# Optimization experiments

Measured on AMD Instinct MI355X. Metric: run time of the kernel, lower is better.

The kernel has to match this reference:

```python
import jax, jax.numpy as jnp
import numpy as np

EPS = 1e-9


def _pairwise_sqdist(x1, x2):
    # x1: (B,n,3), x2: (B,m,3) -> (B,n,m) squared euclidean distances
    s1 = jnp.sum(x1 * x1, axis=-1)
    s2 = jnp.sum(x2 * x2, axis=-1)
    cross = jnp.einsum('bnd,bmd->bnm', x1, x2)
    return jnp.maximum(s1[:, :, None] + s2[:, None, :] - 2.0 * cross, 0.0)


def _approxmatch(x1, x2):
    # Faithful port of the approxmatch CUDA kernel (Fan et al. EMD approx).
    B, n, _ = x1.shape
    m = x2.shape[1]
    if n >= m:
        multiL, multiR = 1.0, float(n // m)   # integer division as in CUDA
    else:
        multiL, multiR = float(m // n), 1.0
    dist = _pairwise_sqdist(x1, x2)  # (B,n,m)
    # j = 7 .. -1 -> level = -4^j ; j = -2 -> level = 0  (10 sweeps total)
    levels = jnp.concatenate([
        -(4.0 ** jnp.arange(7, -2, -1, dtype=jnp.float32)),
        jnp.zeros((1,), jnp.float32)])
    match0 = jnp.zeros((B, n, m), jnp.float32)
    remainL0 = jnp.full((B, n), multiL, jnp.float32)
    remainR0 = jnp.full((B, m), multiR, jnp.float32)

    def body(carry, level):
        match, remainL, remainR = carry
        e = jnp.exp(level * dist)                              # (B,n,m)
        suml = EPS + jnp.einsum('bnm,bm->bn', e, remainR)
        ratioL = remainL / suml                                # (B,n)
        sumr = remainR * jnp.einsum('bnm,bn->bm', e, ratioL)   # (B,m)
        consumption = jnp.minimum(remainR / (sumr + EPS), 1.0)
        ratioR = consumption * remainR                         # (B,m)
        remainR = jnp.maximum(0.0, remainR - sumr)
        w = e * ratioL[:, :, None] * ratioR[:, None, :]        # flow k->l
        match = match + w
        remainL = jnp.maximum(0.0, remainL - jnp.sum(w, axis=-1))
        return (match, remainL, remainR), None

    (match, _, _), _ = jax.lax.scan(body, (match0, remainL0, remainR0), levels)
    return match, dist


def setup_inputs() -> dict:
    key = jax.random.key(0)
    k1, k2 = jax.random.split(key)
    B, N = 4, 4096
    xyz1 = jax.random.normal(k1, (B, 3, N), dtype=jnp.float32)
    xyz2 = jax.random.normal(k2, (B, 3, N), dtype=jnp.float32)
    return {"xyz1": xyz1, "xyz2": xyz2}


def reference(xyz1, xyz2):
    # transpose=True: BCN -> BNC
    x1 = jnp.transpose(xyz1, (0, 2, 1))
    x2 = jnp.transpose(xyz2, (0, 2, 1))
    match, dist = _approxmatch(x1, x2)
    d = jnp.sqrt(jnp.maximum(dist, 1e-20))
    cost = jnp.sum(match * d, axis=(1, 2))            # (B,)
    emd = cost / min(x1.shape[1], x2.shape[1])
    return jnp.mean(emd)                               # reduce_mean=True
```

## Files before the change

kernel.cpp:

```cpp
#include <hip/hip_runtime.h>


#define NPTS 4096
#define BATCH 4
#define EMD_EPS 1e-9f
#define TILE 512
#define RPW 4
#define THREADS 256
#define RPB 16
#define NBLK (NPTS / RPB)
#define NBLK_TOTAL (NBLK * BATCH)

#define GRP_SHIFT 4
#define GRP_SIZE (1 << GRP_SHIFT)
#define NGRP (NBLK_TOTAL / GRP_SIZE)
#define BAR_STRIDE 4352
#define NB_BAR 24

#define CULL_FULL -160.0f
#define CULL_PART -40.0f

typedef float v2f __attribute__((ext_vector_type(2)));

struct Params {
    const float* xyz1;
    const float* xyz2;
    float* remainL;
    float* cost_part;
    float* S_L;
    float* out;
    unsigned* bar;
    float* ratioL[10];
    float* ratioR[9];
    float* remainR[9];
    float ls2[10];
};

struct Smem {
    float4 sA[TILE / 2];
    float4 sB[TILE / 2];
    float2 sC[TILE / 2];
    float  s_cost[THREADS / 64];
};

__device__ __forceinline__ float aload(const float* p_) {
    return __hip_atomic_load((float*)p_, __ATOMIC_RELAXED, __HIP_MEMORY_SCOPE_AGENT);
}
__device__ __forceinline__ void astore(float* p_, float v) {
    __hip_atomic_store(p_, v, __ATOMIC_RELAXED, __HIP_MEMORY_SCOPE_AGENT);
}
__device__ __forceinline__ unsigned au_add(unsigned* p_, unsigned v) {
    return __hip_atomic_fetch_add(p_, v, __ATOMIC_RELAXED, __HIP_MEMORY_SCOPE_AGENT);
}
__device__ __forceinline__ unsigned au_load(const unsigned* p_) {
    return __hip_atomic_load((unsigned*)p_, __ATOMIC_RELAXED, __HIP_MEMORY_SCOPE_AGENT);
}
__device__ __forceinline__ void au_store(unsigned* p_, unsigned v) {
    __hip_atomic_store(p_, v, __ATOMIC_RELAXED, __HIP_MEMORY_SCOPE_AGENT);
}

__device__ __forceinline__ void gsync(unsigned* barbase, int idx) {
    __syncthreads();
    if (threadIdx.x == 0) {
        unsigned* B = barbase + idx * BAR_STRIDE;
        const int bid = blockIdx.y * NBLK + blockIdx.x;
        const int grp = bid >> GRP_SHIFT;
        unsigned* gc   = B + grp * 32;
        unsigned* root = B + NGRP * 32;
        unsigned* gr   = B + NGRP * 32 + 32 + grp * 32;
        unsigned old = au_add(gc, 1u);
        if (old == GRP_SIZE - 1u) {
            unsigned r = au_add(root, 1u) + 1u;
            while (r < (unsigned)NGRP) {
                __builtin_amdgcn_s_sleep(4);
                r = au_load(root);
            }
            au_store(gr, 1u);
        } else {
            while (au_load(gr) == 0u)
                __builtin_amdgcn_s_sleep(4);
        }
        asm volatile("" ::: "memory");
    }
    __syncthreads();
}

__device__ __forceinline__ float fexp2(float x) {
#if __has_builtin(__builtin_amdgcn_exp2f)
    return __builtin_amdgcn_exp2f(x);
#else
    return exp2f(x);
#endif
}
__device__ __forceinline__ float fsqrt(float x) {
#if __has_builtin(__builtin_amdgcn_sqrtf)
    return __builtin_amdgcn_sqrtf(x);
#else
    return __sqrtf(x);
#endif
}

__device__ __forceinline__ float wave_reduce(float v) {
    v += __shfl_xor(v, 32);
    v += __shfl_xor(v, 16);
    v += __shfl_xor(v, 8);
    v += __shfl_xor(v, 4);
    v += __shfl_xor(v, 2);
    v += __shfl_xor(v, 1);
    return v;
}

__device__ __forceinline__ void phase_ratioL0(Smem& sm, const Params& p, float ls2,
                                              float* __restrict__ rLout) {
    const int b = blockIdx.y;
    const int tid = threadIdx.x;
    const int wave = tid >> 6;
    const int lane = tid & 63;
    const int row0 = blockIdx.x * RPB + wave * RPW;

    const float* x1 = p.xyz1 + b * 3 * NPTS;
    const float* x2 = p.xyz2 + b * 3 * NPTS;
    const float2* x2x = (const float2*)(x2);
    const float2* x2y = (const float2*)(x2 + NPTS);
    const float2* x2z = (const float2*)(x2 + 2 * NPTS);

    float px[RPW], py[RPW], pz[RPW];
    v2f acc[RPW];
#pragma unroll
    for (int r = 0; r < RPW; ++r) {
        px[r] = x1[row0 + r];
        py[r] = x1[NPTS + row0 + r];
        pz[r] = x1[2 * NPTS + row0 + r];
        acc[r] = (v2f)(0.0f);
    }
    for (int c0 = 0; c0 < NPTS; c0 += TILE) {
        __syncthreads();
        for (int i = tid; i < TILE / 2; i += THREADS) {
            int e = c0 / 2 + i;
            float2 xx = x2x[e], yy = x2y[e];
            sm.sA[i] = make_float4(xx.x, xx.y, yy.x, yy.y);
            sm.sC[i] = x2z[e];
        }
        __syncthreads();
#pragma unroll 2
        for (int j = 0; j < TILE / 128; ++j) {
            float4 a = sm.sA[lane + 64 * j];
            float2 z = sm.sC[lane + 64 * j];
            v2f ax = {a.x, a.y}, ay = {a.z, a.w}, az = {z.x, z.y};
#pragma unroll
            for (int r = 0; r < RPW; ++r) {
                v2f dx = px[r] - ax, dy = py[r] - ay, dz = pz[r] - az;
                v2f d = dx * dx + dy * dy + dz * dz;
                v2f sd = ls2 * d;
                if (!__all(fmaxf(sd.x, sd.y) < CULL_FULL)) {
                    v2f e2 = {fexp2(sd.x), fexp2(sd.y)};
                    acc[r] += e2;
                }
            }
        }
    }
#pragma unroll
    for (int r = 0; r < RPW; ++r) {
        float s = wave_reduce(acc[r].x + acc[r].y);
        if (lane == 0) {
            int idx = b * NPTS + row0 + r;
            astore(&rLout[idx], 1.0f / (EMD_EPS + s));
            p.remainL[idx] = 1.0f;
        }
    }
}

template <bool CULL>
__device__ __forceinline__ void phase_ratioR(Smem& sm, const Params& p, float ls2,
                                             const float* __restrict__ rL,
                                             const float* __restrict__ rRprev,
                                             float* __restrict__ rRout,
                                             float* __restrict__ remROut) {
    const int b = blockIdx.y;
    const int tid = threadIdx.x;
    const int wave = tid >> 6;
    const int lane = tid & 63;
    const int col0 = blockIdx.x * RPB + wave * RPW;

    const float* x1 = p.xyz1 + b * 3 * NPTS;
    const float* x2 = p.xyz2 + b * 3 * NPTS;
    const float2* x1x = (const float2*)(x1);
    const float2* x1y = (const float2*)(x1 + NPTS);
    const float2* x1z = (const float2*)(x1 + 2 * NPTS);
    const float2* wLv = (const float2*)(rL + b * NPTS);

    float px[RPW], py[RPW], pz[RPW];
    v2f acc[RPW];
#pragma unroll
    for (int r = 0; r < RPW; ++r) {
        px[r] = x2[col0 + r];
        py[r] = x2[NPTS + col0 + r];
        pz[r] = x2[2 * NPTS + col0 + r];
        acc[r] = (v2f)(0.0f);
    }
    for (int c0 = 0; c0 < NPTS; c0 += TILE) {
        __syncthreads();
        for (int i = tid; i < TILE / 2; i += THREADS) {
            int e = c0 / 2 + i;
            float2 xx = x1x[e], yy = x1y[e], zz = x1z[e], ww = wLv[e];
            sm.sA[i] = make_float4(xx.x, xx.y, yy.x, yy.y);
            sm.sB[i] = make_float4(zz.x, zz.y, ww.x, ww.y);
        }
        __syncthreads();
#pragma unroll 2
        for (int j = 0; j < TILE / 128; ++j) {
            float4 a = sm.sA[lane + 64 * j];
            float4 bq = sm.sB[lane + 64 * j];
            v2f ax = {a.x, a.y}, ay = {a.z, a.w};
            v2f az = {bq.x, bq.y}, aw = {bq.z, bq.w};
#pragma unroll
            for (int r = 0; r < RPW; ++r) {
                v2f dx = px[r] - ax, dy = py[r] - ay, dz = pz[r] - az;
                v2f d = dx * dx + dy * dy + dz * dz;
                v2f sd = ls2 * d;
                bool live = true;
                if (CULL) live = !__all(fmaxf(sd.x, sd.y) < CULL_FULL);
                if (live) {
                    v2f e2 = {fexp2(sd.x), fexp2(sd.y)};
                    acc[r] += e2 * aw;
                }
            }
        }
    }
#pragma unroll
    for (int r = 0; r < RPW; ++r) {
        float s = wave_reduce(acc[r].x + acc[r].y);
        if (lane == 0) {
            int idx = b * NPTS + col0 + r;
            float rv = rRprev ? rRprev[idx] : 1.0f;
            float sumr = rv * s;
            float cons = fminf(rv / (sumr + EMD_EPS), 1.0f);
            astore(&rRout[idx], cons * rv);
            astore(&remROut[idx], fmaxf(0.0f, rv - sumr));
        }
    }
}

template <bool SQ, bool CULL>
__device__ __forceinline__ void phase_cost(Smem& sm, const Params& p,
                                           float ls2, float ls2n,
                                           const float* __restrict__ rR,
                                           const float* __restrict__ w2,
                                           const float* __restrict__ rLin,
                                           float* __restrict__ rLout,
                                           int initCost) {
    const int b = blockIdx.y;
    const int tid = threadIdx.x;
    const int wave = tid >> 6;
    const int lane = tid & 63;
    const int row0 = blockIdx.x * RPB + wave * RPW;

    const float* x1 = p.xyz1 + b * 3 * NPTS;
    const float* x2 = p.xyz2 + b * 3 * NPTS;
    const float2* x2x = (const float2*)(x2);
    const float2* x2y = (const float2*)(x2 + NPTS);
    const float2* x2z = (const float2*)(x2 + 2 * NPTS);
    const float2* wRv = (const float2*)(rR + b * NPTS);
    const float2* w2v = (const float2*)(w2 + b * NPTS);

    float px[RPW], py[RPW], pz[RPW];
    v2f acc_a[RPW], acc_c[RPW], acc_s[RPW];
#pragma unroll
    for (int r = 0; r < RPW; ++r) {
        px[r] = x1[row0 + r];
        py[r] = x1[NPTS + row0 + r];
        pz[r] = x1[2 * NPTS + row0 + r];
        acc_a[r] = (v2f)(0.0f);
        acc_c[r] = (v2f)(0.0f);
        acc_s[r] = (v2f)(0.0f);
    }
    for (int c0 = 0; c0 < NPTS; c0 += TILE) {
        __syncthreads();
        for (int i = tid; i < TILE / 2; i += THREADS) {
            int e = c0 / 2 + i;
            float2 xx = x2x[e], yy = x2y[e], zz = x2z[e];
            float2 wr = wRv[e];
            float2 cw = w2v[e];
            sm.sA[i] = make_float4(xx.x, xx.y, yy.x, yy.y);
            sm.sB[i] = make_float4(zz.x, zz.y, wr.x, wr.y);
            sm.sC[i] = cw;
        }
        __syncthreads();
#pragma unroll 2
        for (int j = 0; j < TILE / 128; ++j) {
            float4 a = sm.sA[lane + 64 * j];
            float4 bq = sm.sB[lane + 64 * j];
            float2 c = sm.sC[lane + 64 * j];
            v2f ax = {a.x, a.y}, ay = {a.z, a.w};
            v2f az = {bq.x, bq.y}, wr = {bq.z, bq.w};
            v2f cw = {c.x, c.y};
#pragma unroll
            for (int r = 0; r < RPW; ++r) {
                v2f dx = px[r] - ax, dy = py[r] - ay, dz = pz[r] - az;
                v2f d = dx * dx + dy * dy + dz * dz;
                if (SQ) {
                    v2f sd = ls2n * d;
                    bool fullskip = false, partskip = false;
                    if (CULL) {
                        float mx = fmaxf(sd.x, sd.y);
                        fullskip = __all(mx < CULL_FULL);
                        partskip = __all(mx < CULL_PART);
                    }
                    if (!fullskip) {
                        v2f e2 = {fexp2(sd.x), fexp2(sd.y)};
                        acc_s[r] += e2 * cw;
                        if (!partskip) {
                            v2f e4 = e2 * e2;
                            v2f er = (e4 * e4) * wr;
                            acc_a[r] += er;
                            v2f sq = {fsqrt(d.x), fsqrt(d.y)};
                            acc_c[r] += er * sq;
                        }
                    }
                } else {
                    v2f sd = ls2 * d;
                    v2f e1 = {fexp2(sd.x), fexp2(sd.y)};
                    v2f er = e1 * wr;
                    acc_s[r] += cw;
                    acc_a[r] += er;
                    v2f sq = {fsqrt(d.x), fsqrt(d.y)};
                    acc_c[r] += er * sq;
                }
            }
        }
    }
    float wcost = 0.0f;
#pragma unroll
    for (int r = 0; r < RPW; ++r) {
        float sa = wave_reduce(acc_a[r].x + acc_a[r].y);
        float sc = wave_reduce(acc_c[r].x + acc_c[r].y);
        float ss = wave_reduce(acc_s[r].x + acc_s[r].y);
        if (lane == 0) {
            int idx = b * NPTS + row0 + r;
            float rl = rLin[idx];
            float rem = fmaxf(0.0f, p.remainL[idx] - rl * sa);
            p.remainL[idx] = rem;
            astore(&rLout[idx], rem / (EMD_EPS + ss));
            wcost = fmaf(rl, sc, wcost);
        }
    }
    if (lane == 0) sm.s_cost[wave] = wcost;
    __syncthreads();
    if (tid == 0) {
        float t = sm.s_cost[0] + sm.s_cost[1] + sm.s_cost[2] + sm.s_cost[3];
        int ci = b * NBLK + blockIdx.x;
        astore(&p.cost_part[ci], initCost ? t : aload(&p.cost_part[ci]) + t);
    }
}

__device__ __forceinline__ void phase_sum_ratioL(Smem& sm, const Params& p,
                                                 const float* __restrict__ rL) {
    if (blockIdx.x != 0) return;
    const int b = blockIdx.y;
    const int tid = threadIdx.x;
    float s = 0.0f;
    for (int i = tid; i < NPTS; i += 256) s += rL[b * NPTS + i];
    s = wave_reduce(s);
    if ((tid & 63) == 0) sm.s_cost[tid >> 6] = s;
    __syncthreads();
    if (tid == 0)
        astore(&p.S_L[b], sm.s_cost[0] + sm.s_cost[1] + sm.s_cost[2] + sm.s_cost[3]);
}

__device__ __forceinline__ void phase_cost_l0(Smem& sm, const Params& p,
                                              const float* __restrict__ w2,
                                              const float* __restrict__ rL) {
    const int b = blockIdx.y;
    const int tid = threadIdx.x;
    const int wave = tid >> 6;
    const int lane = tid & 63;
    const int row0 = blockIdx.x * RPB + wave * RPW;
    const float sL = aload(&p.S_L[b]);

    const float* x1 = p.xyz1 + b * 3 * NPTS;
    const float* x2 = p.xyz2 + b * 3 * NPTS;
    const float2* x2x = (const float2*)(x2);
    const float2* x2y = (const float2*)(x2 + NPTS);
    const float2* x2z = (const float2*)(x2 + 2 * NPTS);
    const float2* wRv = (const float2*)(w2 + b * NPTS);

    float px[RPW], py[RPW], pz[RPW];
    v2f acc_c[RPW];
#pragma unroll
    for (int r = 0; r < RPW; ++r) {
        px[r] = x1[row0 + r];
        py[r] = x1[NPTS + row0 + r];
        pz[r] = x1[2 * NPTS + row0 + r];
        acc_c[r] = (v2f)(0.0f);
    }
    for (int c0 = 0; c0 < NPTS; c0 += TILE) {
        __syncthreads();
        for (int i = tid; i < TILE / 2; i += THREADS) {
            int e = c0 / 2 + i;
            float2 xx = x2x[e], yy = x2y[e], zz = x2z[e], rv = wRv[e];
            float wr0 = fminf(rv.x / (rv.x * sL + EMD_EPS), 1.0f) * rv.x;
            float wr1 = fminf(rv.y / (rv.y * sL + EMD_EPS), 1.0f) * rv.y;
            sm.sA[i] = make_float4(xx.x, xx.y, yy.x, yy.y);
            sm.sB[i] = make_float4(zz.x, zz.y, wr0, wr1);
        }
        __syncthreads();
#pragma unroll 2
        for (int j = 0; j < TILE / 128; ++j) {
            float4 a = sm.sA[lane + 64 * j];
            float4 bq = sm.sB[lane + 64 * j];
            v2f ax = {a.x, a.y}, ay = {a.z, a.w};
            v2f az = {bq.x, bq.y}, wr = {bq.z, bq.w};
#pragma unroll
            for (int r = 0; r < RPW; ++r) {
                v2f dx = px[r] - ax, dy = py[r] - ay, dz = pz[r] - az;
                v2f d = dx * dx + dy * dy + dz * dz;
                v2f sq = {fsqrt(d.x), fsqrt(d.y)};
                acc_c[r] += wr * sq;
            }
        }
    }
    float wcost = 0.0f;
#pragma unroll
    for (int r = 0; r < RPW; ++r) {
        float sc = wave_reduce(acc_c[r].x + acc_c[r].y);
        if (lane == 0)
            wcost = fmaf(rL[b * NPTS + row0 + r], sc, wcost);
    }
    if (lane == 0) sm.s_cost[wave] = wcost;
    __syncthreads();
    if (tid == 0) {
        float t = sm.s_cost[0] + sm.s_cost[1] + sm.s_cost[2] + sm.s_cost[3];
        int ci = b * NBLK + blockIdx.x;
        astore(&p.cost_part[ci], aload(&p.cost_part[ci]) + t);
    }
}

__device__ __forceinline__ void phase_final(Smem& sm, const Params& p) {
    if (blockIdx.x != 0 || blockIdx.y != 0) return;
    const int tid = threadIdx.x;
    float s = 0.0f;
    for (int i = tid; i < BATCH * NBLK; i += 256) s += aload(&p.cost_part[i]);
    s = wave_reduce(s);
    if ((tid & 63) == 0) sm.s_cost[tid >> 6] = s;
    __syncthreads();
    if (tid == 0)
        p.out[0] = (sm.s_cost[0] + sm.s_cost[1] + sm.s_cost[2] + sm.s_cost[3]) /
                   ((float)NPTS * (float)BATCH);
}

__global__ __launch_bounds__(THREADS, 4) void k_emd_all(Params p) {
    __shared__ Smem sm;
    int bi = 0;
    phase_ratioL0(sm, p, p.ls2[0], p.ratioL[0]);
    gsync(p.bar, bi++);
    for (int t = 0; t < 9; ++t) {
        const float* rRprev = (t == 0) ? nullptr : p.remainR[t - 1];
        if (t < 4)
            phase_ratioR<true>(sm, p, p.ls2[t], p.ratioL[t], rRprev,
                               p.ratioR[t], p.remainR[t]);
        else
            phase_ratioR<false>(sm, p, p.ls2[t], p.ratioL[t], rRprev,
                                p.ratioR[t], p.remainR[t]);
        gsync(p.bar, bi++);
        if (t < 4)
            phase_cost<true, true>(sm, p, p.ls2[t], p.ls2[t + 1], p.ratioR[t],
                                   p.remainR[t], p.ratioL[t], p.ratioL[t + 1], t == 0);
        else if (t < 8)
            phase_cost<true, false>(sm, p, p.ls2[t], p.ls2[t + 1], p.ratioR[t],
                                    p.remainR[t], p.ratioL[t], p.ratioL[t + 1], 0);
        else
            phase_cost<false, false>(sm, p, p.ls2[8], 0.0f, p.ratioR[8],
                                     p.remainR[8], p.ratioL[8], p.ratioL[9], 0);
        gsync(p.bar, bi++);
    }
    phase_sum_ratioL(sm, p, p.ratioL[9]);
    gsync(p.bar, bi++);
    phase_cost_l0(sm, p, p.remainR[8], p.ratioL[9]);
    gsync(p.bar, bi++);
    phase_final(sm, p);
}

__global__ void k_zero(unsigned* bar) {
    const int n = NB_BAR * BAR_STRIDE;
    for (int i = blockIdx.x * 256 + threadIdx.x; i < n; i += gridDim.x * 256)
        __hip_atomic_store(&bar[i], 0u, __ATOMIC_RELAXED, __HIP_MEMORY_SCOPE_AGENT);
}

__global__ __launch_bounds__(THREADS, 4) void kw_ratioL0(Params p) {
    __shared__ Smem sm;
    phase_ratioL0(sm, p, p.ls2[0], p.ratioL[0]);
}
__global__ __launch_bounds__(THREADS, 4) void kw_ratioR(Params p, int t) {
    __shared__ Smem sm;
    const float* rRprev = (t == 0) ? nullptr : p.remainR[t - 1];
    if (t < 4) phase_ratioR<true>(sm, p, p.ls2[t], p.ratioL[t], rRprev,
                                  p.ratioR[t], p.remainR[t]);
    else       phase_ratioR<false>(sm, p, p.ls2[t], p.ratioL[t], rRprev,
                                   p.ratioR[t], p.remainR[t]);
}
__global__ __launch_bounds__(THREADS, 4) void kw_cost(Params p, int t) {
    __shared__ Smem sm;
    if (t < 4)
        phase_cost<true, true>(sm, p, p.ls2[t], p.ls2[t + 1], p.ratioR[t],
                               p.remainR[t], p.ratioL[t], p.ratioL[t + 1], t == 0);
    else if (t < 8)
        phase_cost<true, false>(sm, p, p.ls2[t], p.ls2[t + 1], p.ratioR[t],
                                p.remainR[t], p.ratioL[t], p.ratioL[t + 1], 0);
    else
        phase_cost<false, false>(sm, p, p.ls2[8], 0.0f, p.ratioR[8],
                                 p.remainR[8], p.ratioL[8], p.ratioL[9], 0);
}
__global__ __launch_bounds__(THREADS, 4) void kw_sum(Params p) {
    __shared__ Smem sm;
    phase_sum_ratioL(sm, p, p.ratioL[9]);
}
__global__ __launch_bounds__(THREADS, 4) void kw_cost_l0(Params p) {
    __shared__ Smem sm;
    phase_cost_l0(sm, p, p.remainR[8], p.ratioL[9]);
}
__global__ __launch_bounds__(THREADS, 4) void kw_final(Params p) {
    __shared__ Smem sm;
    phase_final(sm, p);
}

extern "C" void kernel_launch(void* const* d_in, const int* in_sizes, int n_in,
                              void* d_out, int out_size, void* d_ws, size_t ws_size,
                              hipStream_t stream) {
    Params p;
    p.xyz1 = (const float*)d_in[0];
    p.xyz2 = (const float*)d_in[1];
    const int BN = BATCH * NPTS;
    const int BUF = BN + 1024;
    float* ws = (float*)d_ws;
    p.remainL   = ws;
    p.cost_part = ws + BN;
    p.S_L       = p.cost_part + 2048;
    p.bar       = (unsigned*)(p.S_L + 256);
    float* vbase = (float*)(p.bar + NB_BAR * BAR_STRIDE) + 256;
    for (int t = 0; t < 10; ++t) p.ratioL[t]  = vbase + t * BUF;
    for (int t = 0; t < 9; ++t)  p.ratioR[t]  = vbase + (10 + t) * BUF;
    for (int t = 0; t < 9; ++t)  p.remainR[t] = vbase + (19 + t) * BUF;
    p.out = (float*)d_out;

    static const double levels[10] = {
        -16384.0, -4096.0, -1024.0, -256.0, -64.0,
        -16.0, -4.0, -1.0, -0.25, 0.0};
    for (int t = 0; t < 10; ++t)
        p.ls2[t] = (float)(levels[t] * 1.4426950408889634);

    dim3 grid(NBLK, BATCH), blk(THREADS);

    static int coop_ok = -1;
    if (coop_ok < 0) {
        int v = 0;
        hipDeviceGetAttribute(&v, hipDeviceAttributeCooperativeLaunch, 0);
        coop_ok = v;
    }

    hipError_t err = hipErrorUnknown;
    if (coop_ok) {
        k_zero<<<64, 256, 0, stream>>>(p.bar);
        void* args[] = {(void*)&p};
        err = hipLaunchCooperativeKernel((void*)k_emd_all, grid, blk, args, 0, stream);
    }
    if (err != hipSuccess) {
        kw_ratioL0<<<grid, blk, 0, stream>>>(p);
        for (int t = 0; t < 9; ++t) {
            kw_ratioR<<<grid, blk, 0, stream>>>(p, t);
            kw_cost<<<grid, blk, 0, stream>>>(p, t);
        }
        kw_sum<<<dim3(1, BATCH), blk, 0, stream>>>(p);
        kw_cost_l0<<<grid, blk, 0, stream>>>(p);
        kw_final<<<dim3(1, 1), blk, 0, stream>>>(p);
    }
}
```

Measured before the change: 653.0 us.

## Double-buffer shared-memory tiles with register prefetch in all phases

Converts each phase's tile loop to a double-buffered scheme. The next tile's global loads go into registers before computing on the current shared-memory buffer, then the registers are written to the alternate buffer. This hides global load latency behind the exp/sqrt compute and drops one of the two barriers per tile. In exchange it doubles shared memory use and adds register pressure, which may lower occupancy. Its correctness depends on TILE/2 equalling THREADS, since each thread now loads exactly one element.

```diff
diff --git a/kernel.cpp b/kernel.cpp
--- a/kernel.cpp
+++ b/kernel.cpp
@@ -5,6 +5,7 @@
 #define BATCH 4
 #define EMD_EPS 1e-9f
 #define TILE 512
+#define NTILE (NPTS / TILE)
 #define RPW 4
 #define THREADS 256
 #define RPB 16
@@ -37,9 +38,9 @@
 };
 
 struct Smem {
-    float4 sA[TILE / 2];
-    float4 sB[TILE / 2];
-    float2 sC[TILE / 2];
+    float4 sA[2][TILE / 2];
+    float4 sB[2][TILE / 2];
+    float2 sC[2][TILE / 2];
     float  s_cost[THREADS / 64];
 };
 
@@ -133,19 +134,24 @@
         pz[r] = x1[2 * NPTS + row0 + r];
         acc[r] = (v2f)(0.0f);
     }
-    for (int c0 = 0; c0 < NPTS; c0 += TILE) {
-        __syncthreads();
-        for (int i = tid; i < TILE / 2; i += THREADS) {
-            int e = c0 / 2 + i;
-            float2 xx = x2x[e], yy = x2y[e];
-            sm.sA[i] = make_float4(xx.x, xx.y, yy.x, yy.y);
-            sm.sC[i] = x2z[e];
-        }
-        __syncthreads();
+    float2 g0, g1, g2;
+    {
+        int e = tid;
+        g0 = x2x[e]; g1 = x2y[e]; g2 = x2z[e];
+        sm.sA[0][tid] = make_float4(g0.x, g0.y, g1.x, g1.y);
+        sm.sC[0][tid] = g2;
+    }
+    __syncthreads();
+    for (int kt = 0; kt < NTILE; ++kt) {
+        const int cur = kt & 1;
+        if (kt + 1 < NTILE) {
+            int e = (kt + 1) * (TILE / 2) + tid;
+            g0 = x2x[e]; g1 = x2y[e]; g2 = x2z[e];
+        }
 #pragma unroll 2
         for (int j = 0; j < TILE / 128; ++j) {
-            float4 a = sm.sA[lane + 64 * j];
-            float2 z = sm.sC[lane + 64 * j];
+            float4 a = sm.sA[cur][lane + 64 * j];
+            float2 z = sm.sC[cur][lane + 64 * j];
             v2f ax = {a.x, a.y}, ay = {a.z, a.w}, az = {z.x, z.y};
 #pragma unroll
             for (int r = 0; r < RPW; ++r) {
@@ -157,6 +163,11 @@
                     acc[r] += e2;
                 }
             }
+        }
+        if (kt + 1 < NTILE) {
+            sm.sA[cur ^ 1][tid] = make_float4(g0.x, g0.y, g1.x, g1.y);
+            sm.sC[cur ^ 1][tid] = g2;
+            __syncthreads();
         }
     }
 #pragma unroll
@@ -198,19 +209,24 @@
         pz[r] = x2[2 * NPTS + col0 + r];
         acc[r] = (v2f)(0.0f);
     }
-    for (int c0 = 0; c0 < NPTS; c0 += TILE) {
-        __syncthreads();
-        for (int i = tid; i < TILE / 2; i += THREADS) {
-            int e = c0 / 2 + i;
-            float2 xx = x1x[e], yy = x1y[e], zz = x1z[e], ww = wLv[e];
-            sm.sA[i] = make_float4(xx.x, xx.y, yy.x, yy.y);
-            sm.sB[i] = make_float4(zz.x, zz.y, ww.x, ww.y);
-        }
-        __syncthreads();
+    float2 g0, g1, g2, g3;
+    {
+        int e = tid;
+        g0 = x1x[e]; g1 = x1y[e]; g2 = x1z[e]; g3 = wLv[e];
+        sm.sA[0][tid] = make_float4(g0.x, g0.y, g1.x, g1.y);
+        sm.sB[0][tid] = make_float4(g2.x, g2.y, g3.x, g3.y);
+    }
+    __syncthreads();
+    for (int kt = 0; kt < NTILE; ++kt) {
+        const int cur = kt & 1;
+        if (kt + 1 < NTILE) {
+            int e = (kt + 1) * (TILE / 2) + tid;
+            g0 = x1x[e]; g1 = x1y[e]; g2 = x1z[e]; g3 = wLv[e];
+        }
 #pragma unroll 2
         for (int j = 0; j < TILE / 128; ++j) {
-            float4 a = sm.sA[lane + 64 * j];
-            float4 bq = sm.sB[lane + 64 * j];
+            float4 a = sm.sA[cur][lane + 64 * j];
+            float4 bq = sm.sB[cur][lane + 64 * j];
             v2f ax = {a.x, a.y}, ay = {a.z, a.w};
             v2f az = {bq.x, bq.y}, aw = {bq.z, bq.w};
 #pragma unroll
@@ -225,6 +241,11 @@
                     acc[r] += e2 * aw;
                 }
             }
+        }
+        if (kt + 1 < NTILE) {
+            sm.sA[cur ^ 1][tid] = make_float4(g0.x, g0.y, g1.x, g1.y);
+            sm.sB[cur ^ 1][tid] = make_float4(g2.x, g2.y, g3.x, g3.y);
+            __syncthreads();
         }
     }
 #pragma unroll
@@ -274,23 +295,26 @@
         acc_c[r] = (v2f)(0.0f);
         acc_s[r] = (v2f)(0.0f);
     }
-    for (int c0 = 0; c0 < NPTS; c0 += TILE) {
-        __syncthreads();
-        for (int i = tid; i < TILE / 2; i += THREADS) {
-            int e = c0 / 2 + i;
-            float2 xx = x2x[e], yy = x2y[e], zz = x2z[e];
-            float2 wr = wRv[e];
-            float2 cw = w2v[e];
-            sm.sA[i] = make_float4(xx.x, xx.y, yy.x, yy.y);
-            sm.sB[i] = make_float4(zz.x, zz.y, wr.x, wr.y);
-            sm.sC[i] = cw;
-        }
-        __syncthreads();
+    float2 g0, g1, g2, g3, g4;
+    {
+        int e = tid;
+        g0 = x2x[e]; g1 = x2y[e]; g2 = x2z[e]; g3 = wRv[e]; g4 = w2v[e];
+        sm.sA[0][tid] = make_float4(g0.x, g0.y, g1.x, g1.y);
+        sm.sB[0][tid] = make_float4(g2.x, g2.y, g3.x, g3.y);
+        sm.sC[0][tid] = g4;
+    }
+    __syncthreads();
+    for (int kt = 0; kt < NTILE; ++kt) {
+        const int cur = kt & 1;
+        if (kt + 1 < NTILE) {
+            int e = (kt + 1) * (TILE / 2) + tid;
+            g0 = x2x[e]; g1 = x2y[e]; g2 = x2z[e]; g3 = wRv[e]; g4 = w2v[e];
+        }
 #pragma unroll 2
         for (int j = 0; j < TILE / 128; ++j) {
-            float4 a = sm.sA[lane + 64 * j];
-            float4 bq = sm.sB[lane + 64 * j];
-            float2 c = sm.sC[lane + 64 * j];
+            float4 a = sm.sA[cur][lane + 64 * j];
+            float4 bq = sm.sB[cur][lane + 64 * j];
+            float2 c = sm.sC[cur][lane + 64 * j];
             v2f ax = {a.x, a.y}, ay = {a.z, a.w};
             v2f az = {bq.x, bq.y}, wr = {bq.z, bq.w};
             v2f cw = {c.x, c.y};
@@ -328,6 +352,12 @@
                 }
             }
         }
+        if (kt + 1 < NTILE) {
+            sm.sA[cur ^ 1][tid] = make_float4(g0.x, g0.y, g1.x, g1.y);
+            sm.sB[cur ^ 1][tid] = make_float4(g2.x, g2.y, g3.x, g3.y);
+            sm.sC[cur ^ 1][tid] = g4;
+            __syncthreads();
+        }
     }
     float wcost = 0.0f;
 #pragma unroll
@@ -393,21 +423,26 @@
         pz[r] = x1[2 * NPTS + row0 + r];
         acc_c[r] = (v2f)(0.0f);
     }
-    for (int c0 = 0; c0 < NPTS; c0 += TILE) {
-        __syncthreads();
-        for (int i = tid; i < TILE / 2; i += THREADS) {
-            int e = c0 / 2 + i;
-            float2 xx = x2x[e], yy = x2y[e], zz = x2z[e], rv = wRv[e];
-            float wr0 = fminf(rv.x / (rv.x * sL + EMD_EPS), 1.0f) * rv.x;
-            float wr1 = fminf(rv.y / (rv.y * sL + EMD_EPS), 1.0f) * rv.y;
-            sm.sA[i] = make_float4(xx.x, xx.y, yy.x, yy.y);
-            sm.sB[i] = make_float4(zz.x, zz.y, wr0, wr1);
-        }
-        __syncthreads();
+    float2 g0, g1, g2, g3;
+    {
+        int e = tid;
+        g0 = x2x[e]; g1 = x2y[e]; g2 = x2z[e]; g3 = wRv[e];
+        float wr0 = fminf(g3.x / (g3.x * sL + EMD_EPS), 1.0f) * g3.x;
+        float wr1 = fminf(g3.y / (g3.y * sL + EMD_EPS), 1.0f) * g3.y;
+        sm.sA[0][tid] = make_float4(g0.x, g0.y, g1.x, g1.y);
+        sm.sB[0][tid] = make_float4(g2.x, g2.y, wr0, wr1);
+    }
+    __syncthreads();
+    for (int kt = 0; kt < NTILE; ++kt) {
+        const int cur = kt & 1;
+        if (kt + 1 < NTILE) {
+            int e = (kt + 1) * (TILE / 2) + tid;
+            g0 = x2x[e]; g1 = x2y[e]; g2 = x2z[e]; g3 = wRv[e];
+        }
 #pragma unroll 2
         for (int j = 0; j < TILE / 128; ++j) {
-            float4 a = sm.sA[lane + 64 * j];
-            float4 bq = sm.sB[lane + 64 * j];
+            float4 a = sm.sA[cur][lane + 64 * j];
+            float4 bq = sm.sB[cur][lane + 64 * j];
             v2f ax = {a.x, a.y}, ay = {a.z, a.w};
             v2f az = {bq.x, bq.y}, wr = {bq.z, bq.w};
 #pragma unroll
@@ -417,6 +452,13 @@
                 v2f sq = {fsqrt(d.x), fsqrt(d.y)};
                 acc_c[r] += wr * sq;
             }
+        }
+        if (kt + 1 < NTILE) {
+            float wr0 = fminf(g3.x / (g3.x * sL + EMD_EPS), 1.0f) * g3.x;
+            float wr1 = fminf(g3.y / (g3.y * sL + EMD_EPS), 1.0f) * g3.y;
+            sm.sA[cur ^ 1][tid] = make_float4(g0.x, g0.y, g1.x, g1.y);
+            sm.sB[cur ^ 1][tid] = make_float4(g2.x, g2.y, wr0, wr1);
+            __syncthreads();
         }
     }
     float wcost = 0.0f;
```

New measurement: 695.4 us. +6.5%, slower.
